# Optimization experiments

Measured on AMD Instinct MI355X. Metric: run time of the kernel, lower is better.

The kernel has to match this reference:

```python
import jax, jax.numpy as jnp
import numpy as np

B, N, M, R = 128, 511, 256, 64
IN = 512  # word_dim + tag_dim


def setup_inputs() -> dict:
    key = jax.random.key(0)
    ks = jax.random.split(key, 16)
    def w(k, shape, fan_in):
        return jax.random.normal(k, shape, dtype=jnp.float32) / np.sqrt(fan_in)
    inp = {
        "word_tag_emb": jax.random.normal(ks[0], (B, N, IN), dtype=jnp.float32),
        "rel_emb": jax.random.normal(ks[1], (B, N, R), dtype=jnp.float32),
        "n_nodes": N,
    }
    for j, nm in enumerate(["ix", "fx", "ux", "ox"]):
        inp["W" + nm] = w(ks[2 + j], (IN, M), IN)
        inp["b" + nm] = jnp.zeros((M,), jnp.float32)
    for j, nm in enumerate(["ih", "fh", "uh", "oh"]):
        inp["W" + nm] = w(ks[6 + j], (M, M), M)
        inp["b" + nm] = jnp.zeros((M,), jnp.float32)
    # seq_lstm (nn.LSTM, 1 layer): gate order i, f, g, o; stored [in, 4M]
    inp["W_seq_ih"] = w(ks[10], (M + R, 4 * M), M + R)
    inp["W_seq_hh"] = w(ks[11], (M, 4 * M), M)
    inp["b_seq_ih"] = jnp.zeros((4 * M,), jnp.float32)
    inp["b_seq_hh"] = jnp.zeros((4 * M,), jnp.float32)
    return inp


def reference(word_tag_emb, rel_emb,
              Wix, bix, Wfx, bfx, Wux, bux, Wox, box,
              Wih, bih, Wfh, bfh, Wuh, buh, Woh, boh,
              W_seq_ih, W_seq_hh, b_seq_ih, b_seq_hh, n_nodes):
    Bn, Nn, _ = word_tag_emb.shape
    Mm = Wih.shape[0]
    dt = word_tag_emb.dtype

    def lstm_cell(x, h, c):
        g = x @ W_seq_ih + h @ W_seq_hh + (b_seq_ih + b_seq_hh)
        i, f, gg, o = jnp.split(g, 4, axis=-1)
        c2 = jax.nn.sigmoid(f) * c + jax.nn.sigmoid(i) * jnp.tanh(gg)
        return jax.nn.sigmoid(o) * jnp.tanh(c2), c2

    def step(carry, node):
        h_buf, c_buf = carry  # [B, N, M] state buffers
        ch = jnp.stack([2 * node + 1, 2 * node + 2])        # heap children
        valid = (ch < Nn).astype(dt)[:, None, None]          # [2,1,1]
        idx = jnp.minimum(ch, Nn - 1)
        ch_h = jnp.take(h_buf, idx, axis=1).transpose(1, 0, 2) * valid   # [2,B,M]
        ch_c = jnp.take(c_buf, idx, axis=1).transpose(1, 0, 2) * valid   # [2,B,M]
        ch_r = jnp.take(rel_emb, idx, axis=1).transpose(1, 0, 2) * valid # [2,B,R]
        # seq_lstm over the (masked) child sequence: input [h_j ; rel_j]
        hs = jnp.zeros((Bn, Mm), dt)
        cs = jnp.zeros((Bn, Mm), dt)
        for j in range(2):  # fixed max_children (binary tree)
            hn, cn = lstm_cell(jnp.concatenate([ch_h[j], ch_r[j]], -1), hs, cs)
            hs = valid[j] * hn + (1.0 - valid[j]) * hs
            cs = valid[j] * cn + (1.0 - valid[j]) * cs
        h_tilde = hs  # stays zero at leaves (seq_lstm never run there)
        x = word_tag_emb[:, node]  # [B, IN]
        i = jax.nn.sigmoid(x @ Wix + bix + h_tilde @ Wih + bih)
        o = jax.nn.sigmoid(x @ Wox + box + h_tilde @ Woh + boh)
        u = jnp.tanh(x @ Wux + bux + h_tilde @ Wuh + buh)
        f = jax.nn.sigmoid((x @ Wfx + bfx)[None] + ch_h @ Wfh + bfh)  # [2,B,M]
        c = i * u + jnp.sum(f * ch_c * valid, axis=0)
        h = o * jnp.tanh(c)
        h_buf = h_buf.at[:, node].set(h)
        c_buf = c_buf.at[:, node].set(c)
        return (h_buf, c_buf), None

    h0 = jnp.zeros((Bn, Nn, Mm), dt)
    c0 = jnp.zeros((Bn, Nn, Mm), dt)
    nodes = jnp.arange(Nn - 1, -1, -1)  # bottom-up (children before parents)
    (h_buf, c_buf), _ = jax.lax.scan(step, (h0, c0), nodes)
    return h_buf[:, 0]  # root hidden state, [B, M]
```

## Files before the change

### kernel.cpp

```cpp
#include <hip/hip_runtime.h>
#include <math.h>

#define NNODE 511

typedef short s16x8 __attribute__((ext_vector_type(8)));
typedef float f32x4 __attribute__((ext_vector_type(4)));

__device__ __forceinline__ unsigned short f2bf(float f) {
  unsigned int u = __builtin_bit_cast(unsigned int, f);
  u += 0x7fffu + ((u >> 16) & 1u);
  return (unsigned short)(u >> 16);
}
__device__ __forceinline__ float sigf(float x) {
  float e = __builtin_amdgcn_exp2f(-1.442695040888963f * x);
  return __builtin_amdgcn_rcpf(1.0f + e);
}
__device__ __forceinline__ float tanh_a(float x) {
  float e = __builtin_amdgcn_exp2f(2.885390081777927f * x);
  return 1.0f - 2.0f * __builtin_amdgcn_rcpf(1.0f + e);
}

__device__ __forceinline__ void load16_lds(const unsigned short* g, unsigned short* l) {
  __builtin_amdgcn_global_load_lds(
      (const __attribute__((address_space(1))) void*)g,
      (__attribute__((address_space(3))) void*)l, 16, 0, 0);
}

template<int N> __device__ __forceinline__ void s_wait_vmcnt() {
  asm volatile("s_waitcnt vmcnt(%0)" :: "n"(N) : "memory");
}

__device__ __forceinline__ void swz_blk(int& bx, int& by) {
  bx = blockIdx.x; by = blockIdx.y;
  int ny = gridDim.y;
  if ((ny & 7) == 0) {
    int lin = by * 8 + bx;
    int w = lin >> 3;
    by = (lin & 7) * (ny >> 3) + (w >> 3);
    bx = w & 7;
  }
}

__global__ void k_prep_x(const float* __restrict__ w, unsigned short* __restrict__ xbf) {
  int o = (blockIdx.x * 256 + threadIdx.x) * 4;
  int node = o >> 16;
  int b = (o >> 9) & 127;
  int k = o & 511;
  const float4 v = *(const float4*)(w + ((size_t)b * NNODE + node) * 512 + k);
  unsigned int p0 = (unsigned int)f2bf(v.x) | ((unsigned int)f2bf(v.y) << 16);
  unsigned int p1 = (unsigned int)f2bf(v.z) | ((unsigned int)f2bf(v.w) << 16);
  *(uint2*)(xbf + o) = make_uint2(p0, p1);
}

__global__ void k_prep_w(const float* __restrict__ Wix, const float* __restrict__ Wux,
                         const float* __restrict__ Wox, const float* __restrict__ Wfx,
                         const float* __restrict__ Wih, const float* __restrict__ Wuh,
                         const float* __restrict__ Woh, const float* __restrict__ Wfh,
                         const float* __restrict__ Wsi, const float* __restrict__ Wsh,
                         unsigned short* __restrict__ WL2t, unsigned short* __restrict__ WA2t,
                         unsigned short* __restrict__ WG2t, unsigned short* __restrict__ WEX2t) {
  int idx = blockIdx.x * 256 + threadIdx.x;
  if (idx < 393216) {
    int c = idx >> 9, k = idx & 511;
    int G = c / 48, rem = c - G * 48, g = rem >> 4, mi = rem & 15, m = G * 16 + mi;
    const float* W = (g == 0) ? Wix : (g == 1) ? Wux : Wox;
    WL2t[idx] = f2bf(W[k * 256 + m]);
  } else if (idx < 802816) {
    int o = idx - 393216;
    int c = o / 320, k = o - c * 320;
    int G = c / 80, rem = c - G * 80, g = rem >> 4, mi = rem & 15, m = G * 16 + mi;
    float v;
    if (g < 4) v = Wsi[k * 1024 + g * 256 + m];
    else       v = (k < 256) ? Wfh[k * 256 + m] : 0.0f;
    WA2t[o] = f2bf(v);
  } else if (idx < 1540096) {
    int o = idx - 802816;
    int c = o / 576, k = o - c * 576;
    int G = c / 80, rem = c - G * 80, g = rem >> 4, mi = rem & 15, m = G * 16 + mi;
    float v;
    if (g < 4) v = (k < 256) ? Wsh[k * 1024 + g * 256 + m]
                             : Wsi[(k - 256) * 1024 + g * 256 + m];
    else       v = (k >= 256 && k < 512) ? Wfh[(k - 256) * 256 + m] : 0.0f;
    WG2t[o] = f2bf(v);
  } else if (idx < 2326528) {
    int o = idx - 1540096;
    int c = o / 768, k = o - c * 768;
    int G = c >> 6, rem = c & 63, g = rem >> 4, mi = rem & 15, m = G * 16 + mi;
    float v;
    if (k < 256) {
      v = (g == 0) ? Wih[k * 256 + m] : (g == 1) ? Wuh[k * 256 + m]
        : (g == 2) ? Woh[k * 256 + m] : 0.0f;
    } else {
      int k2 = k - 256;
      v = (g == 0) ? Wix[k2 * 256 + m] : (g == 1) ? Wux[k2 * 256 + m]
        : (g == 2) ? Wox[k2 * 256 + m] : Wfx[k2 * 256 + m];
    }
    WEX2t[o] = f2bf(v);
  }
}

#define MFMA_BODY(AP, BP, NG, CW)                                             \
  _Pragma("unroll")                                                           \
  for (int kk = 0; kk < 64; kk += 32) {                                       \
    const int sw = (kk | (q * 8)) ^ ((m16 & 7) * 8);                          \
    s16x8 af[4], bfr[NG];                                                     \
    _Pragma("unroll")                                                         \
    for (int i = 0; i < 4; ++i)                                               \
      af[i] = *(const s16x8*)(&(AP)[(wm + i * 16 + m16) * 64 + sw]);          \
    _Pragma("unroll")                                                         \
    for (int j = 0; j < NG; ++j)                                              \
      bfr[j] = *(const s16x8*)(&(BP)[(wc * CW + j * 16 + m16) * 64 + sw]);    \
    _Pragma("unroll")                                                         \
    for (int i = 0; i < 4; ++i)                                               \
      _Pragma("unroll")                                                       \
      for (int j = 0; j < NG; ++j)                                            \
        acc[i][j] = __builtin_amdgcn_mfma_f32_16x16x32_bf16(af[i], bfr[j], acc[i][j], 0, 0, 0); \
  }

#define STAGE(DST, SRC, STRIDE, R, K0)                                        \
  _Pragma("unroll")                                                           \
  for (int c = 0; c < (R) / 32; ++c) {                                        \
    int row8 = wave * ((R) / 4) + c * 8;                                      \
    load16_lds(SRC + (size_t)(row8 + l8) * (STRIDE) + (K0) + gsw, &(DST)[row8 * 64]); \
  }

#define STEP_SYNC(VM)                                                         \
  s_wait_vmcnt<VM>();                                                         \
  __builtin_amdgcn_s_barrier();                                               \
  __builtin_amdgcn_sched_barrier(0);

__global__ __launch_bounds__(256, 2) void k_gemm1(
    const unsigned short* __restrict__ AinL, const unsigned short* __restrict__ Bt,
    unsigned short* __restrict__ h1, float* __restrict__ c1,
    float* __restrict__ FHL,
    const float* __restrict__ bsi, const float* __restrict__ bsh) {
  __shared__ alignas(16) unsigned short As[2][128 * 64];
  __shared__ alignas(16) unsigned short Bs[2][160 * 64];
  int bx, by; swz_blk(bx, by);
  const int t = threadIdx.x;
  const int wave = t >> 6, lane = t & 63;
  const int wm = (wave & 1) * 64, wc = wave >> 1;
  const int m16 = lane & 15, q = lane >> 4;
  const int l8 = lane >> 3, l7 = lane & 7;
  const int gsw = ((l7 ^ l8) * 8);
  const int rowBase = by * 128;
  const unsigned short* Arow = AinL + (size_t)rowBase * 320;
  const unsigned short* Brow = Bt + (size_t)bx * 160 * 320;
  f32x4 acc[4][5] = {};
  const int m = (bx * 2 + wc) * 16 + m16;

  float bi = bsi[m] + bsh[m];
  float bg = bsi[512 + m] + bsh[512 + m];
  float bo = bsi[768 + m] + bsh[768 + m];

  STAGE(As[0], Arow, 320, 128, 0)
  STAGE(Bs[0], Brow, 320, 160, 0)
#pragma unroll
  for (int ti = 0; ti < 5; ++ti) {
    if (ti < 4) {
      STAGE(As[(ti + 1) & 1], Arow, 320, 128, (ti + 1) * 64)
      STAGE(Bs[(ti + 1) & 1], Brow, 320, 160, (ti + 1) * 64)
      STEP_SYNC(9)
    } else {
      STEP_SYNC(0)
    }
    MFMA_BODY(As[ti & 1], Bs[ti & 1], 5, 80)
    __builtin_amdgcn_s_barrier();
  }

#pragma unroll
  for (int i = 0; i < 4; ++i)
#pragma unroll
    for (int r2 = 0; r2 < 4; ++r2) {
      int r = rowBase + wm + i * 16 + q * 4 + r2;
      float ii = sigf(acc[i][0][r2] + bi);
      float gg = tanh_a(acc[i][2][r2] + bg);
      float oo = sigf(acc[i][3][r2] + bo);
      float cv = ii * gg;
      size_t o = (size_t)r * 256 + m;
      h1[o] = f2bf(oo * tanh_a(cv));
      c1[o] = cv;
      FHL[o] = acc[i][4][r2];
    }
}

__global__ __launch_bounds__(256, 2) void k_gemm2(
    const unsigned short* __restrict__ h1, const unsigned short* __restrict__ AinR,
    const unsigned short* __restrict__ Bt,
    const float* __restrict__ c1, unsigned short* __restrict__ HT,
    float* __restrict__ FHR,
    const float* __restrict__ bsi, const float* __restrict__ bsh) {
  __shared__ alignas(16) unsigned short As[2][128 * 64];
  __shared__ alignas(16) unsigned short Bs[2][160 * 64];
  int bx, by; swz_blk(bx, by);
  const int t = threadIdx.x;
  const int wave = t >> 6, lane = t & 63;
  const int wm = (wave & 1) * 64, wc = wave >> 1;
  const int m16 = lane & 15, q = lane >> 4;
  const int l8 = lane >> 3, l7 = lane & 7;
  const int gsw = ((l7 ^ l8) * 8);
  const int rowBase = by * 128;
  const unsigned short* Brow = Bt + (size_t)bx * 160 * 576;
  f32x4 acc[4][5] = {};
  const int m = (bx * 2 + wc) * 16 + m16;

  float b0 = bsi[m] + bsh[m];
  float b1 = bsi[256 + m] + bsh[256 + m];
  float b2 = bsi[512 + m] + bsh[512 + m];
  float b3 = bsi[768 + m] + bsh[768 + m];

  float pc[4][4];

  auto stageA = [&](unsigned short* dst, int kb) {
    if (kb < 256) {
      const unsigned short* Arow = h1 + (size_t)rowBase * 256;
#pragma unroll
      for (int c = 0; c < 4; ++c) {
        int row8 = wave * 32 + c * 8;
        load16_lds(Arow + (size_t)(row8 + l8) * 256 + kb + gsw, &dst[row8 * 64]);
      }
    } else {
      const unsigned short* Arow = AinR + (size_t)rowBase * 320;
      int k0 = kb - 256;
#pragma unroll
      for (int c = 0; c < 4; ++c) {
        int row8 = wave * 32 + c * 8;
        load16_lds(Arow + (size_t)(row8 + l8) * 320 + k0 + gsw, &dst[row8 * 64]);
      }
    }
  };

  stageA(As[0], 0);
  STAGE(Bs[0], Brow, 576, 160, 0)
#pragma unroll
  for (int ti = 0; ti < 9; ++ti) {
    if (ti < 8) {
      stageA(As[(ti + 1) & 1], (ti + 1) * 64);
      STAGE(Bs[(ti + 1) & 1], Brow, 576, 160, (ti + 1) * 64)
      STEP_SYNC(9)
      if (ti == 7) {
#pragma unroll
        for (int i = 0; i < 4; ++i)
#pragma unroll
          for (int r2 = 0; r2 < 4; ++r2) {
            int r = rowBase + wm + i * 16 + q * 4 + r2;
            pc[i][r2] = c1[(size_t)r * 256 + m];
          }
      }
    } else {
      STEP_SYNC(16)
    }
    MFMA_BODY(As[ti & 1], Bs[ti & 1], 5, 80)
    __builtin_amdgcn_s_barrier();
  }

#pragma unroll
  for (int i = 0; i < 4; ++i)
#pragma unroll
    for (int r2 = 0; r2 < 4; ++r2) {
      int r = rowBase + wm + i * 16 + q * 4 + r2;
      size_t o = (size_t)r * 256 + m;
      float ii = sigf(acc[i][0][r2] + b0);
      float ff = sigf(acc[i][1][r2] + b1);
      float gg = tanh_a(acc[i][2][r2] + b2);
      float oo = sigf(acc[i][3][r2] + b3);
      float c2 = ff * pc[i][r2] + ii * gg;
      HT[o] = f2bf(oo * tanh_a(c2));
      FHR[o] = acc[i][4][r2];
    }
}

__global__ __launch_bounds__(256, 2) void k_gemm3(
    const unsigned short* __restrict__ HT, const unsigned short* __restrict__ xnode,
    const unsigned short* __restrict__ Bt,
    const float* __restrict__ FHL, const float* __restrict__ FHR,
    float* __restrict__ cbuf, unsigned short* __restrict__ Ain,
    const float* __restrict__ rel, float* __restrict__ out,
    const float* __restrict__ bix, const float* __restrict__ bih,
    const float* __restrict__ bux, const float* __restrict__ buh,
    const float* __restrict__ box, const float* __restrict__ boh,
    const float* __restrict__ bfx, const float* __restrict__ bfh,
    int base, int v0, int n, int lvl) {
  __shared__ alignas(16) unsigned short As[2][128 * 64];
  __shared__ alignas(16) unsigned short Bs[2][128 * 64];
  int bx, by; swz_blk(bx, by);
  const int t = threadIdx.x;
  const int wave = t >> 6, lane = t & 63;
  const int wm = (wave & 1) * 64, wc = wave >> 1;
  const int m16 = lane & 15, q = lane >> 4;
  const int l8 = lane >> 3, l7 = lane & 7;
  const int gsw = ((l7 ^ l8) * 8);
  const int rowBase = by * 128;
  const unsigned short* Brow = Bt + (size_t)bx * 128 * 768;
  f32x4 acc[4][4] = {};
  const int m = (bx * 2 + wc) * 16 + m16;

  float bi = bix[m] + bih[m];
  float bu = bux[m] + buh[m];
  float bo = box[m] + boh[m];
  float bf = bfx[m] + bfh[m];

  float pfl[4][4], pfr[4][4], pc0[4][4], pc1v[4][4];

  auto stageA = [&](unsigned short* dst, int kb) {
    if (kb < 256) {
      const unsigned short* Arow = HT + (size_t)rowBase * 256;
#pragma unroll
      for (int c = 0; c < 4; ++c) {
        int row8 = wave * 32 + c * 8;
        load16_lds(Arow + (size_t)(row8 + l8) * 256 + kb + gsw, &dst[row8 * 64]);
      }
    } else {
      const unsigned short* Arow = xnode + (size_t)rowBase * 512;
      int k0 = kb - 256;
#pragma unroll
      for (int c = 0; c < 4; ++c) {
        int row8 = wave * 32 + c * 8;
        load16_lds(Arow + (size_t)(row8 + l8) * 512 + k0 + gsw, &dst[row8 * 64]);
      }
    }
  };

  stageA(As[0], 0);
  STAGE(Bs[0], Brow, 768, 128, 0)
#pragma unroll
  for (int ti = 0; ti < 12; ++ti) {
    if (ti < 11) {
      stageA(As[(ti + 1) & 1], (ti + 1) * 64);
      STAGE(Bs[(ti + 1) & 1], Brow, 768, 128, (ti + 1) * 64)
      STEP_SYNC(8)
      if (ti == 10) {
#pragma unroll
        for (int i = 0; i < 4; ++i)
#pragma unroll
          for (int r2 = 0; r2 < 4; ++r2) {
            int r = rowBase + wm + i * 16 + q * 4 + r2;
            int b = r & 127;
            int node = base + v0 + (r >> 7);
            size_t o = (size_t)r * 256 + m;
            size_t co = ((size_t)(2 * node + 1) * 128 + b) * 256 + m;
            pfl[i][r2] = FHL[o];
            pfr[i][r2] = FHR[o];
            pc0[i][r2] = cbuf[co];
            pc1v[i][r2] = cbuf[co + 32768];
          }
      }
    } else {
      STEP_SYNC(63)
    }
    MFMA_BODY(As[ti & 1], Bs[ti & 1], 4, 64)
    __builtin_amdgcn_s_barrier();
  }

#pragma unroll
  for (int i = 0; i < 4; ++i)
#pragma unroll
    for (int r2 = 0; r2 < 4; ++r2) {
      int r = rowBase + wm + i * 16 + q * 4 + r2;
      int vloc = r >> 7, b = r & 127;
      int vg = v0 + vloc;
      int node = base + vg;
      float pf = acc[i][3][r2] + bf;
      float f0 = sigf(pf + pfl[i][r2]);
      float f1 = sigf(pf + pfr[i][r2]);
      float ii = sigf(acc[i][0][r2] + bi);
      float uu = tanh_a(acc[i][1][r2] + bu);
      float oo = sigf(acc[i][2][r2] + bo);
      float cc = ii * uu + f0 * pc0[i][r2] + f1 * pc1v[i][r2];
      float hh = oo * tanh_a(cc);
      if (lvl == 0) {
        out[b * 256 + m] = hh;
      } else {
        cbuf[((size_t)node * 128 + b) * 256 + m] = cc;
        int rowA = (vg & 1) * (n >> 1) * 128 + (vg >> 1) * 128 + b;
        Ain[(size_t)rowA * 320 + m] = f2bf(hh);
        if (m < 64)
          Ain[(size_t)rowA * 320 + 256 + m] = f2bf(rel[((size_t)b * NNODE + node) * 64 + m]);
      }
    }
}

__global__ __launch_bounds__(256, 2) void k_leaf(
    const unsigned short* __restrict__ xleaf, const unsigned short* __restrict__ Bt,
    float* __restrict__ cbuf, unsigned short* __restrict__ Ain,
    const float* __restrict__ rel,
    const float* __restrict__ bix, const float* __restrict__ bih,
    const float* __restrict__ bux, const float* __restrict__ buh,
    const float* __restrict__ box, const float* __restrict__ boh) {
  __shared__ alignas(16) unsigned short As[2][128 * 64];
  __shared__ alignas(16) unsigned short Bs[2][96 * 64];
  int bx, by; swz_blk(bx, by);
  const int t = threadIdx.x;
  const int wave = t >> 6, lane = t & 63;
  const int wm = (wave & 1) * 64, wc = wave >> 1;
  const int m16 = lane & 15, q = lane >> 4;
  const int l8 = lane >> 3, l7 = lane & 7;
  const int gsw = ((l7 ^ l8) * 8);
  const int rowBase = by * 128;
  const unsigned short* Arow = xleaf + (size_t)rowBase * 512;
  const unsigned short* Brow = Bt + (size_t)bx * 96 * 512;
  f32x4 acc[4][3] = {};
  const int m = (bx * 2 + wc) * 16 + m16;

  float bi = bix[m] + bih[m];
  float bu = bux[m] + buh[m];
  float bo = box[m] + boh[m];

  STAGE(As[0], Arow, 512, 128, 0)
#pragma unroll
  for (int c = 0; c < 3; ++c) {
    int row8 = wave * 24 + c * 8;
    load16_lds(Brow + (size_t)(row8 + l8) * 512 + 0 + gsw, &Bs[0][row8 * 64]);
  }
#pragma unroll
  for (int ti = 0; ti < 8; ++ti) {
    if (ti < 7) {
      int kn = (ti + 1) * 64;
      STAGE(As[(ti + 1) & 1], Arow, 512, 128, kn)
#pragma unroll
      for (int c = 0; c < 3; ++c) {
        int row8 = wave * 24 + c * 8;
        load16_lds(Brow + (size_t)(row8 + l8) * 512 + kn + gsw, &Bs[(ti + 1) & 1][row8 * 64]);
      }
      STEP_SYNC(7)
    } else {
      STEP_SYNC(0)
    }
    MFMA_BODY(As[ti & 1], Bs[ti & 1], 3, 48)
    __builtin_amdgcn_s_barrier();
  }

#pragma unroll
  for (int i = 0; i < 4; ++i)
#pragma unroll
    for (int r2 = 0; r2 < 4; ++r2) {
      int r = rowBase + wm + i * 16 + q * 4 + r2;
      int vg = r >> 7, b = r & 127;
      int node = 255 + vg;
      float ii = sigf(acc[i][0][r2] + bi);
      float uu = tanh_a(acc[i][1][r2] + bu);
      float oo = sigf(acc[i][2][r2] + bo);
      float cc = ii * uu;
      float hh = oo * tanh_a(cc);
      cbuf[((size_t)node * 128 + b) * 256 + m] = cc;
      int rowA = (vg & 1) * 16384 + (vg >> 1) * 128 + b;
      Ain[(size_t)rowA * 320 + m] = f2bf(hh);
      if (m < 64)
        Ain[(size_t)rowA * 320 + 256 + m] = f2bf(rel[((size_t)b * NNODE + node) * 64 + m]);
    }
}

extern "C" void kernel_launch(void* const* d_in, const int* in_sizes, int n_in,
                              void* d_out, int out_size, void* d_ws, size_t ws_size,
                              hipStream_t stream) {
  const float* wte = (const float*)d_in[0];
  const float* rel = (const float*)d_in[1];
  const float* Wix = (const float*)d_in[3];
  const float* bix = (const float*)d_in[4];
  const float* Wfx = (const float*)d_in[5];
  const float* bfx = (const float*)d_in[6];
  const float* Wux = (const float*)d_in[7];
  const float* bux = (const float*)d_in[8];
  const float* Wox = (const float*)d_in[9];
  const float* box = (const float*)d_in[10];
  const float* Wih = (const float*)d_in[11];
  const float* bih = (const float*)d_in[12];
  const float* Wfh = (const float*)d_in[13];
  const float* bfh = (const float*)d_in[14];
  const float* Wuh = (const float*)d_in[15];
  const float* buh = (const float*)d_in[16];
  const float* Woh = (const float*)d_in[17];
  const float* boh = (const float*)d_in[18];
  const float* Wsi = (const float*)d_in[19];
  const float* Wsh = (const float*)d_in[20];
  const float* bsi = (const float*)d_in[21];
  const float* bsh = (const float*)d_in[22];
  float* out = (float*)d_out;
  (void)in_sizes; (void)n_in; (void)out_size;

  int INT_MAXN;
  if (ws_size >= (size_t)310 * 1024 * 1024)      INT_MAXN = 128;
  else if (ws_size >= (size_t)200 * 1024 * 1024) INT_MAXN = 32;
  else                                           INT_MAXN = 8;
  const int crowsMax = INT_MAXN * 128;

  char* ws = (char*)d_ws;
  size_t off = 0;
  auto alloc = [&](size_t bytes) {
    size_t o = off; off += (bytes + 255) & ~(size_t)255; return o;
  };
  unsigned short* xbf  = (unsigned short*)(ws + alloc((size_t)NNODE * 128 * 512 * 2));
  float*          cbuf = (float*)         (ws + alloc((size_t)NNODE * 128 * 256 * 4));
  unsigned short* Ain  = (unsigned short*)(ws + alloc((size_t)32768 * 320 * 2));
  unsigned short* WL2t = (unsigned short*)(ws + alloc((size_t)768 * 512 * 2));
  unsigned short* WA2t = (unsigned short*)(ws + alloc((size_t)1280 * 320 * 2));
  unsigned short* WG2t = (unsigned short*)(ws + alloc((size_t)1280 * 576 * 2));
  unsigned short* WEX2t= (unsigned short*)(ws + alloc((size_t)1024 * 768 * 2));
  unsigned short* h1   = (unsigned short*)(ws + alloc((size_t)crowsMax * 256 * 2));
  float*          c1   = (float*)         (ws + alloc((size_t)crowsMax * 256 * 4));
  float*          FHL  = (float*)         (ws + alloc((size_t)crowsMax * 256 * 4));
  float*          FHR  = (float*)         (ws + alloc((size_t)crowsMax * 256 * 4));
  unsigned short* HT   = (unsigned short*)(ws + alloc((size_t)crowsMax * 256 * 2));

  k_prep_x<<<32704, 256, 0, stream>>>(wte, xbf);
  k_prep_w<<<9088, 256, 0, stream>>>(Wix, Wux, Wox, Wfx, Wih, Wuh, Woh, Wfh,
                                     Wsi, Wsh, WL2t, WA2t, WG2t, WEX2t);

  k_leaf<<<dim3(8, 256), 256, 0, stream>>>(xbf + (size_t)255 * 128 * 512, WL2t,
                                           cbuf, Ain, rel, bix, bih, bux, buh, box, boh);

  for (int lvl = 7; lvl >= 0; --lvl) {
    int n = 1 << lvl;
    int base = n - 1;
    int cn = (n < INT_MAXN) ? n : INT_MAXN;
    for (int v0 = 0; v0 < n; v0 += cn) {
      const unsigned short* AinL = Ain + (size_t)(v0 * 128) * 320;
      const unsigned short* AinR = Ain + (size_t)((n + v0) * 128) * 320;
      const unsigned short* xnode = xbf + (size_t)(base + v0) * 128 * 512;
      k_gemm1<<<dim3(8, cn), 256, 0, stream>>>(AinL, WA2t, h1, c1, FHL, bsi, bsh);
      k_gemm2<<<dim3(8, cn), 256, 0, stream>>>(h1, AinR, WG2t, c1, HT, FHR, bsi, bsh);
      k_gemm3<<<dim3(8, cn), 256, 0, stream>>>(HT, xnode, WEX2t, FHL, FHR, cbuf, Ain,
                                               rel, out, bix, bih, bux, buh, box, boh,
                                               bfx, bfh, base, v0, n, lvl);
    }
  }
}
```

Baseline: 742.5 us.

## Fuse top five tree levels into one persistent kernel with grid barriers

Replaces the per-level gemm1/gemm2/gemm3 launches for levels 4..0 with a single persistent kernel, k_tail, of 8x16 blocks. It synchronizes between phases with an atomic grid-wide barrier, which removes around fifteen small kernel launches and their launch gaps on the serial tail of the tree. It also makes k_leaf process four row tiles per block, prefetching across tiles and shrinking its grid. The risks are that the spin barrier depends on all 128 blocks being resident at once, and that most blocks sit idle at the small top levels.

```diff
diff --git a/kernel.cpp b/kernel.cpp
--- a/kernel.cpp
+++ b/kernel.cpp
@@ -41,7 +41,28 @@
   }
 }
 
-__global__ void k_prep_x(const float* __restrict__ w, unsigned short* __restrict__ xbf) {
+__device__ __forceinline__ void gridbar(unsigned* cnt, unsigned* gen) {
+  __syncthreads();
+  if (threadIdx.x == 0) {
+    __threadfence();
+    unsigned nb = gridDim.x * gridDim.y;
+    unsigned g = __hip_atomic_load(gen, __ATOMIC_RELAXED, __HIP_MEMORY_SCOPE_AGENT);
+    unsigned a = __hip_atomic_fetch_add(cnt, 1u, __ATOMIC_ACQ_REL, __HIP_MEMORY_SCOPE_AGENT);
+    if (a == nb - 1u) {
+      __hip_atomic_store(cnt, 0u, __ATOMIC_RELAXED, __HIP_MEMORY_SCOPE_AGENT);
+      __hip_atomic_fetch_add(gen, 1u, __ATOMIC_RELEASE, __HIP_MEMORY_SCOPE_AGENT);
+    } else {
+      while (__hip_atomic_load(gen, __ATOMIC_ACQUIRE, __HIP_MEMORY_SCOPE_AGENT) == g) {
+        __builtin_amdgcn_s_sleep(2);
+      }
+    }
+  }
+  __syncthreads();
+}
+
+__global__ void k_prep_x(const float* __restrict__ w, unsigned short* __restrict__ xbf,
+                         unsigned* __restrict__ bar) {
+  if (blockIdx.x == 0 && threadIdx.x == 0) { bar[0] = 0u; bar[1] = 0u; }
   int o = (blockIdx.x * 256 + threadIdx.x) * 4;
   int node = o >> 16;
   int b = (o >> 9) & 127;
@@ -129,6 +150,14 @@
   __builtin_amdgcn_s_barrier();                                               \
   __builtin_amdgcn_sched_barrier(0);
 
+#define LANE_SETUP                                                            \
+  const int t = threadIdx.x;                                                  \
+  const int wave = t >> 6, lane = t & 63;                                     \
+  const int wm = (wave & 1) * 64, wc = wave >> 1;                             \
+  const int m16 = lane & 15, q = lane >> 4;                                   \
+  const int l8 = lane >> 3, l7 = lane & 7;                                    \
+  const int gsw = ((l7 ^ l8) * 8);
+
 __global__ __launch_bounds__(256, 2) void k_gemm1(
     const unsigned short* __restrict__ AinL, const unsigned short* __restrict__ Bt,
     unsigned short* __restrict__ h1, float* __restrict__ c1,
@@ -137,12 +166,7 @@
   __shared__ alignas(16) unsigned short As[2][128 * 64];
   __shared__ alignas(16) unsigned short Bs[2][160 * 64];
   int bx, by; swz_blk(bx, by);
-  const int t = threadIdx.x;
-  const int wave = t >> 6, lane = t & 63;
-  const int wm = (wave & 1) * 64, wc = wave >> 1;
-  const int m16 = lane & 15, q = lane >> 4;
-  const int l8 = lane >> 3, l7 = lane & 7;
-  const int gsw = ((l7 ^ l8) * 8);
+  LANE_SETUP
   const int rowBase = by * 128;
   const unsigned short* Arow = AinL + (size_t)rowBase * 320;
   const unsigned short* Brow = Bt + (size_t)bx * 160 * 320;
@@ -193,12 +217,7 @@
   __shared__ alignas(16) unsigned short As[2][128 * 64];
   __shared__ alignas(16) unsigned short Bs[2][160 * 64];
   int bx, by; swz_blk(bx, by);
-  const int t = threadIdx.x;
-  const int wave = t >> 6, lane = t & 63;
-  const int wm = (wave & 1) * 64, wc = wave >> 1;
-  const int m16 = lane & 15, q = lane >> 4;
-  const int l8 = lane >> 3, l7 = lane & 7;
-  const int gsw = ((l7 ^ l8) * 8);
+  LANE_SETUP
   const int rowBase = by * 128;
   const unsigned short* Brow = Bt + (size_t)bx * 160 * 576;
   f32x4 acc[4][5] = {};
@@ -284,12 +303,7 @@
   __shared__ alignas(16) unsigned short As[2][128 * 64];
   __shared__ alignas(16) unsigned short Bs[2][128 * 64];
   int bx, by; swz_blk(bx, by);
-  const int t = threadIdx.x;
-  const int wave = t >> 6, lane = t & 63;
-  const int wm = (wave & 1) * 64, wc = wave >> 1;
-  const int m16 = lane & 15, q = lane >> 4;
-  const int l8 = lane >> 3, l7 = lane & 7;
-  const int gsw = ((l7 ^ l8) * 8);
+  LANE_SETUP
   const int rowBase = by * 128;
   const unsigned short* Brow = Bt + (size_t)bx * 128 * 768;
   f32x4 acc[4][4] = {};
@@ -390,64 +404,265 @@
   __shared__ alignas(16) unsigned short As[2][128 * 64];
   __shared__ alignas(16) unsigned short Bs[2][96 * 64];
   int bx, by; swz_blk(bx, by);
-  const int t = threadIdx.x;
-  const int wave = t >> 6, lane = t & 63;
-  const int wm = (wave & 1) * 64, wc = wave >> 1;
-  const int m16 = lane & 15, q = lane >> 4;
-  const int l8 = lane >> 3, l7 = lane & 7;
-  const int gsw = ((l7 ^ l8) * 8);
-  const int rowBase = by * 128;
-  const unsigned short* Arow = xleaf + (size_t)rowBase * 512;
+  LANE_SETUP
+  const int RT = 4;
   const unsigned short* Brow = Bt + (size_t)bx * 96 * 512;
-  f32x4 acc[4][3] = {};
   const int m = (bx * 2 + wc) * 16 + m16;
 
   float bi = bix[m] + bih[m];
   float bu = bux[m] + buh[m];
   float bo = box[m] + boh[m];
 
-  STAGE(As[0], Arow, 512, 128, 0)
-#pragma unroll
-  for (int c = 0; c < 3; ++c) {
-    int row8 = wave * 24 + c * 8;
-    load16_lds(Brow + (size_t)(row8 + l8) * 512 + 0 + gsw, &Bs[0][row8 * 64]);
-  }
-#pragma unroll
-  for (int ti = 0; ti < 8; ++ti) {
-    if (ti < 7) {
-      int kn = (ti + 1) * 64;
-      STAGE(As[(ti + 1) & 1], Arow, 512, 128, kn)
-#pragma unroll
-      for (int c = 0; c < 3; ++c) {
-        int row8 = wave * 24 + c * 8;
-        load16_lds(Brow + (size_t)(row8 + l8) * 512 + kn + gsw, &Bs[(ti + 1) & 1][row8 * 64]);
-      }
-      STEP_SYNC(7)
-    } else {
-      STEP_SYNC(0)
-    }
-    MFMA_BODY(As[ti & 1], Bs[ti & 1], 3, 48)
-    __builtin_amdgcn_s_barrier();
-  }
-
-#pragma unroll
-  for (int i = 0; i < 4; ++i)
-#pragma unroll
-    for (int r2 = 0; r2 < 4; ++r2) {
-      int r = rowBase + wm + i * 16 + q * 4 + r2;
-      int vg = r >> 7, b = r & 127;
-      int node = 255 + vg;
-      float ii = sigf(acc[i][0][r2] + bi);
-      float uu = tanh_a(acc[i][1][r2] + bu);
-      float oo = sigf(acc[i][2][r2] + bo);
-      float cc = ii * uu;
-      float hh = oo * tanh_a(cc);
-      cbuf[((size_t)node * 128 + b) * 256 + m] = cc;
-      int rowA = (vg & 1) * 16384 + (vg >> 1) * 128 + b;
-      Ain[(size_t)rowA * 320 + m] = f2bf(hh);
-      if (m < 64)
-        Ain[(size_t)rowA * 320 + 256 + m] = f2bf(rel[((size_t)b * NNODE + node) * 64 + m]);
-    }
+  {
+    const unsigned short* Arow = xleaf + (size_t)(by * RT) * 128 * 512;
+    STAGE(As[0], Arow, 512, 128, 0)
+#pragma unroll
+    for (int c = 0; c < 3; ++c) {
+      int row8 = wave * 24 + c * 8;
+      load16_lds(Brow + (size_t)(row8 + l8) * 512 + 0 + gsw, &Bs[0][row8 * 64]);
+    }
+  }
+
+  for (int r = 0; r < RT; ++r) {
+    const int ty = by * RT + r;
+    const unsigned short* Arow = xleaf + (size_t)ty * 128 * 512;
+    const unsigned short* ArowN = xleaf + (size_t)(ty + 1) * 128 * 512;
+    f32x4 acc[4][3] = {};
+#pragma unroll
+    for (int ti = 0; ti < 8; ++ti) {
+      if (ti < 7) {
+        int kn = (ti + 1) * 64;
+        STAGE(As[(ti + 1) & 1], Arow, 512, 128, kn)
+#pragma unroll
+        for (int c = 0; c < 3; ++c) {
+          int row8 = wave * 24 + c * 8;
+          load16_lds(Brow + (size_t)(row8 + l8) * 512 + kn + gsw, &Bs[(ti + 1) & 1][row8 * 64]);
+        }
+        STEP_SYNC(7)
+      } else if (r + 1 < RT) {
+        STAGE(As[0], ArowN, 512, 128, 0)
+#pragma unroll
+        for (int c = 0; c < 3; ++c) {
+          int row8 = wave * 24 + c * 8;
+          load16_lds(Brow + (size_t)(row8 + l8) * 512 + 0 + gsw, &Bs[0][row8 * 64]);
+        }
+        STEP_SYNC(7)
+      } else {
+        STEP_SYNC(0)
+      }
+      MFMA_BODY(As[ti & 1], Bs[ti & 1], 3, 48)
+      __builtin_amdgcn_s_barrier();
+    }
+
+#pragma unroll
+    for (int i = 0; i < 4; ++i)
+#pragma unroll
+      for (int r2 = 0; r2 < 4; ++r2) {
+        int lr = wm + i * 16 + q * 4 + r2;
+        int b = lr;
+        int node = 255 + ty;
+        float ii = sigf(acc[i][0][r2] + bi);
+        float uu = tanh_a(acc[i][1][r2] + bu);
+        float oo = sigf(acc[i][2][r2] + bo);
+        float cc = ii * uu;
+        float hh = oo * tanh_a(cc);
+        cbuf[((size_t)node * 128 + b) * 256 + m] = cc;
+        int rowA = (ty & 1) * 16384 + (ty >> 1) * 128 + b;
+        Ain[(size_t)rowA * 320 + m] = f2bf(hh);
+        if (m < 64)
+          Ain[(size_t)rowA * 320 + 256 + m] = f2bf(rel[((size_t)b * NNODE + node) * 64 + m]);
+      }
+  }
+}
+
+__global__ __launch_bounds__(256, 2) void k_tail(
+    unsigned short* __restrict__ Ain, const unsigned short* __restrict__ xbf,
+    const unsigned short* __restrict__ WA2t, const unsigned short* __restrict__ WG2t,
+    const unsigned short* __restrict__ WEX2t,
+    unsigned short* __restrict__ h1, float* __restrict__ c1,
+    float* __restrict__ FHL, float* __restrict__ FHR,
+    unsigned short* __restrict__ HT, float* __restrict__ cbuf,
+    const float* __restrict__ rel, float* __restrict__ out,
+    const float* __restrict__ bsi, const float* __restrict__ bsh,
+    const float* __restrict__ bix, const float* __restrict__ bih,
+    const float* __restrict__ bux, const float* __restrict__ buh,
+    const float* __restrict__ box, const float* __restrict__ boh,
+    const float* __restrict__ bfx, const float* __restrict__ bfh,
+    unsigned* __restrict__ bar) {
+  __shared__ alignas(16) unsigned short As[2][128 * 64];
+  __shared__ alignas(16) unsigned short Bs[2][160 * 64];
+  const int bx = blockIdx.x, by = blockIdx.y;
+  LANE_SETUP
+  const int m = (bx * 2 + wc) * 16 + m16;
+
+  for (int lvl = 4; lvl >= 0; --lvl) {
+    const int n = 1 << lvl;
+    const int base = n - 1;
+
+    if (by < n) {
+      const unsigned short* Arow = Ain + (size_t)by * 128 * 320;
+      const unsigned short* Brow = WA2t + (size_t)bx * 160 * 320;
+      float bi = bsi[m] + bsh[m];
+      float bg = bsi[512 + m] + bsh[512 + m];
+      float bo = bsi[768 + m] + bsh[768 + m];
+      f32x4 acc[4][5] = {};
+      STAGE(As[0], Arow, 320, 128, 0)
+      STAGE(Bs[0], Brow, 320, 160, 0)
+#pragma unroll
+      for (int ti = 0; ti < 5; ++ti) {
+        if (ti < 4) {
+          STAGE(As[(ti + 1) & 1], Arow, 320, 128, (ti + 1) * 64)
+          STAGE(Bs[(ti + 1) & 1], Brow, 320, 160, (ti + 1) * 64)
+          STEP_SYNC(9)
+        } else {
+          STEP_SYNC(0)
+        }
+        MFMA_BODY(As[ti & 1], Bs[ti & 1], 5, 80)
+        __builtin_amdgcn_s_barrier();
+      }
+#pragma unroll
+      for (int i = 0; i < 4; ++i)
+#pragma unroll
+        for (int r2 = 0; r2 < 4; ++r2) {
+          int r = by * 128 + wm + i * 16 + q * 4 + r2;
+          float ii = sigf(acc[i][0][r2] + bi);
+          float gg = tanh_a(acc[i][2][r2] + bg);
+          float oo = sigf(acc[i][3][r2] + bo);
+          float cv = ii * gg;
+          size_t o = (size_t)r * 256 + m;
+          h1[o] = f2bf(oo * tanh_a(cv));
+          c1[o] = cv;
+          FHL[o] = acc[i][4][r2];
+        }
+    }
+    gridbar(bar, bar + 1);
+
+    if (by < n) {
+      const unsigned short* Brow = WG2t + (size_t)bx * 160 * 576;
+      float b0 = bsi[m] + bsh[m];
+      float b1 = bsi[256 + m] + bsh[256 + m];
+      float b2 = bsi[512 + m] + bsh[512 + m];
+      float b3 = bsi[768 + m] + bsh[768 + m];
+      f32x4 acc[4][5] = {};
+      auto stA = [&](unsigned short* dst, int kb) {
+        if (kb < 256) {
+          const unsigned short* Arow = h1 + (size_t)by * 128 * 256;
+#pragma unroll
+          for (int c = 0; c < 4; ++c) {
+            int row8 = wave * 32 + c * 8;
+            load16_lds(Arow + (size_t)(row8 + l8) * 256 + kb + gsw, &dst[row8 * 64]);
+          }
+        } else {
+          const unsigned short* Arow = Ain + (size_t)(n + by) * 128 * 320;
+          int k0 = kb - 256;
+#pragma unroll
+          for (int c = 0; c < 4; ++c) {
+            int row8 = wave * 32 + c * 8;
+            load16_lds(Arow + (size_t)(row8 + l8) * 320 + k0 + gsw, &dst[row8 * 64]);
+          }
+        }
+      };
+      stA(As[0], 0);
+      STAGE(Bs[0], Brow, 576, 160, 0)
+#pragma unroll
+      for (int ti = 0; ti < 9; ++ti) {
+        if (ti < 8) {
+          stA(As[(ti + 1) & 1], (ti + 1) * 64);
+          STAGE(Bs[(ti + 1) & 1], Brow, 576, 160, (ti + 1) * 64)
+          STEP_SYNC(9)
+        } else {
+          STEP_SYNC(0)
+        }
+        MFMA_BODY(As[ti & 1], Bs[ti & 1], 5, 80)
+        __builtin_amdgcn_s_barrier();
+      }
+#pragma unroll
+      for (int i = 0; i < 4; ++i)
+#pragma unroll
+        for (int r2 = 0; r2 < 4; ++r2) {
+          int r = by * 128 + wm + i * 16 + q * 4 + r2;
+          size_t o = (size_t)r * 256 + m;
+          float ii = sigf(acc[i][0][r2] + b0);
+          float ff = sigf(acc[i][1][r2] + b1);
+          float gg = tanh_a(acc[i][2][r2] + b2);
+          float oo = sigf(acc[i][3][r2] + b3);
+          float c2 = ff * c1[o] + ii * gg;
+          HT[o] = f2bf(oo * tanh_a(c2));
+          FHR[o] = acc[i][4][r2];
+        }
+    }
+    gridbar(bar, bar + 1);
+
+    if (by < n) {
+      const unsigned short* xnode = xbf + (size_t)base * 128 * 512;
+      const unsigned short* Brow = WEX2t + (size_t)bx * 128 * 768;
+      float bi = bix[m] + bih[m];
+      float bu = bux[m] + buh[m];
+      float bo = box[m] + boh[m];
+      float bf = bfx[m] + bfh[m];
+      f32x4 acc[4][4] = {};
+      auto stA = [&](unsigned short* dst, int kb) {
+        if (kb < 256) {
+          const unsigned short* Arow = HT + (size_t)by * 128 * 256;
+#pragma unroll
+          for (int c = 0; c < 4; ++c) {
+            int row8 = wave * 32 + c * 8;
+            load16_lds(Arow + (size_t)(row8 + l8) * 256 + kb + gsw, &dst[row8 * 64]);
+          }
+        } else {
+          const unsigned short* Arow = xnode + (size_t)by * 128 * 512;
+          int k0 = kb - 256;
+#pragma unroll
+          for (int c = 0; c < 4; ++c) {
+            int row8 = wave * 32 + c * 8;
+            load16_lds(Arow + (size_t)(row8 + l8) * 512 + k0 + gsw, &dst[row8 * 64]);
+          }
+        }
+      };
+      stA(As[0], 0);
+      STAGE(Bs[0], Brow, 768, 128, 0)
+#pragma unroll
+      for (int ti = 0; ti < 12; ++ti) {
+        if (ti < 11) {
+          stA(As[(ti + 1) & 1], (ti + 1) * 64);
+          STAGE(Bs[(ti + 1) & 1], Brow, 768, 128, (ti + 1) * 64)
+          STEP_SYNC(8)
+        } else {
+          STEP_SYNC(0)
+        }
+        MFMA_BODY(As[ti & 1], Bs[ti & 1], 4, 64)
+        __builtin_amdgcn_s_barrier();
+      }
+#pragma unroll
+      for (int i = 0; i < 4; ++i)
+#pragma unroll
+        for (int r2 = 0; r2 < 4; ++r2) {
+          int lr = wm + i * 16 + q * 4 + r2;
+          int b = lr;
+          int node = base + by;
+          size_t o = (size_t)(by * 128 + lr) * 256 + m;
+          size_t co = ((size_t)(2 * node + 1) * 128 + b) * 256 + m;
+          float pf = acc[i][3][r2] + bf;
+          float f0 = sigf(pf + FHL[o]);
+          float f1 = sigf(pf + FHR[o]);
+          float ii = sigf(acc[i][0][r2] + bi);
+          float uu = tanh_a(acc[i][1][r2] + bu);
+          float oo = sigf(acc[i][2][r2] + bo);
+          float cc = ii * uu + f0 * cbuf[co] + f1 * cbuf[co + 32768];
+          float hh = oo * tanh_a(cc);
+          if (lvl == 0) {
+            out[b * 256 + m] = hh;
+          } else {
+            cbuf[((size_t)node * 128 + b) * 256 + m] = cc;
+            int rowA = (by & 1) * (n >> 1) * 128 + (by >> 1) * 128 + b;
+            Ain[(size_t)rowA * 320 + m] = f2bf(hh);
+            if (m < 64)
+              Ain[(size_t)rowA * 320 + 256 + m] = f2bf(rel[((size_t)b * NNODE + node) * 64 + m]);
+          }
+        }
+    }
+    if (lvl > 0) gridbar(bar, bar + 1);
+  }
 }
 
 extern "C" void kernel_launch(void* const* d_in, const int* in_sizes, int n_in,
@@ -501,15 +716,18 @@
   float*          FHL  = (float*)         (ws + alloc((size_t)crowsMax * 256 * 4));
   float*          FHR  = (float*)         (ws + alloc((size_t)crowsMax * 256 * 4));
   unsigned short* HT   = (unsigned short*)(ws + alloc((size_t)crowsMax * 256 * 2));
-
-  k_prep_x<<<32704, 256, 0, stream>>>(wte, xbf);
+  unsigned*       bar  = (unsigned*)      (ws + alloc(256));
+
+  k_prep_x<<<32704, 256, 0, stream>>>(wte, xbf, bar);
   k_prep_w<<<9088, 256, 0, stream>>>(Wix, Wux, Wox, Wfx, Wih, Wuh, Woh, Wfh,
                                      Wsi, Wsh, WL2t, WA2t, WG2t, WEX2t);
 
-  k_leaf<<<dim3(8, 256), 256, 0, stream>>>(xbf + (size_t)255 * 128 * 512, WL2t,
-                                           cbuf, Ain, rel, bix, bih, bux, buh, box, boh);
-
-  for (int lvl = 7; lvl >= 0; --lvl) {
+  k_leaf<<<dim3(8, 64), 256, 0, stream>>>(xbf + (size_t)255 * 128 * 512, WL2t,
+                                          cbuf, Ain, rel, bix, bih, bux, buh, box, boh);
+
+  const bool fuse = (INT_MAXN >= 16);
+  const int lvlMin = fuse ? 5 : 0;
+  for (int lvl = 7; lvl >= lvlMin; --lvl) {
     int n = 1 << lvl;
     int base = n - 1;
     int cn = (n < INT_MAXN) ? n : INT_MAXN;
@@ -524,4 +742,10 @@
                                                bfx, bfh, base, v0, n, lvl);
     }
   }
-}
+  if (fuse) {
+    k_tail<<<dim3(8, 16), 256, 0, stream>>>(Ain, xbf, WA2t, WG2t, WEX2t,
+                                            h1, c1, FHL, FHR, HT, cbuf, rel, out,
+                                            bsi, bsh, bix, bih, bux, buh, box, boh,
+                                            bfx, bfh, bar);
+  }
+}
```

Measured after the change: 1.828 ms. +146.2%, slower.
